# Kernel optimization log

Measured on AMD Instinct MI355X. Metric: run time of the kernel, lower is better.

## Reference

```python
import jax, jax.numpy as jnp
import numpy as np

N_NODES = 100000
N_EDGES = 300000
NUM_GRAPHS = 2000
IN_DIM = 82
HIDDEN = 256


def _gcn_conv(x, src, dst, dinv, W, b):
    # GCNConv: out = D^-1/2 (A + I) D^-1/2 (x W) + b
    xW = x @ W  # [N, H]
    norm = dinv[src] * dinv[dst]  # [E]
    agg = jax.ops.segment_sum(xW[src] * norm[:, None], dst, num_segments=N_NODES)
    self_loop = xW * (dinv * dinv)[:, None]
    return agg + self_loop + b


def setup_inputs() -> dict:
    key = jax.random.key(0)
    ks = jax.random.split(key, 8)
    x = jax.random.normal(ks[0], (N_NODES, IN_DIM), dtype=jnp.float32)
    edge_index = jax.random.randint(ks[1], (2, N_EDGES), 0, N_NODES, dtype=jnp.int64)
    batch = jnp.sort(jax.random.randint(ks[2], (N_NODES,), 0, NUM_GRAPHS, dtype=jnp.int64))
    W1 = jax.random.normal(ks[3], (IN_DIM, HIDDEN), dtype=jnp.float32) * (1.0 / np.sqrt(IN_DIM))
    W2 = jax.random.normal(ks[4], (HIDDEN, HIDDEN), dtype=jnp.float32) * (1.0 / np.sqrt(HIDDEN))
    W3 = jax.random.normal(ks[5], (HIDDEN, HIDDEN), dtype=jnp.float32) * (1.0 / np.sqrt(HIDDEN))
    b1 = jnp.zeros((HIDDEN,), jnp.float32)
    b2 = jnp.zeros((HIDDEN,), jnp.float32)
    b3 = jnp.zeros((HIDDEN,), jnp.float32)
    return {"x": x, "edge_index": edge_index, "batch": batch, "num_graphs": NUM_GRAPHS,
            "W1": W1, "b1": b1, "W2": W2, "b2": b2, "W3": W3, "b3": b3}


def reference(x, edge_index, batch, num_graphs, W1, b1, W2, b2, W3, b3):
    src, dst = edge_index[0], edge_index[1]
    # symmetric normalization with added self-loops (PyG gcn_norm)
    deg = jax.ops.segment_sum(jnp.ones_like(dst, dtype=x.dtype), dst, num_segments=N_NODES) + 1.0
    dinv = jax.lax.rsqrt(deg)
    h = jax.nn.relu(_gcn_conv(x, src, dst, dinv, W1, b1))
    h = jax.nn.relu(_gcn_conv(h, src, dst, dinv, W2, b2))
    h = jax.nn.relu(_gcn_conv(h, src, dst, dinv, W3, b3))
    return jax.ops.segment_max(h, batch, num_segments=num_graphs)  # [G, H]
```

## Files before the change

kernel.cpp:

```cpp
#include <hip/hip_runtime.h>
#include <cstdint>
#include <cstddef>

#define N_NODES 100000
#define N_EDGES 300000
#define N_GRAPHS 2000
#define HID 256
#define INDIM 82
#define K1PAD 96
#define SCAN_CHUNK 2048
#define NBLK_SCAN ((N_NODES + SCAN_CHUNK - 1) / SCAN_CHUNK)

typedef __bf16 bf16x8 __attribute__((ext_vector_type(8)));
typedef float f32x4 __attribute__((ext_vector_type(4)));

__device__ __forceinline__ unsigned short f2bf(float f) {
    unsigned int u = __float_as_uint(f);
    u = (u + 0x7fffu + ((u >> 16) & 1u)) >> 16;
    return (unsigned short)u;
}
__device__ __forceinline__ float bf2f(unsigned short s) {
    return __uint_as_float(((unsigned int)s) << 16);
}

__global__ void k_cnt_init(int* cnt) {
    int i = blockIdx.x * 256 + threadIdx.x;
    if (i < N_NODES) cnt[i] = 0;
}

__global__ void k_cnt_acc(const int* __restrict__ ei, int* cnt) {
    int e = blockIdx.x * 256 + threadIdx.x;
    if (e < N_EDGES) atomicAdd(&cnt[ei[N_EDGES + e]], 1);
}

__global__ void k_dinv(const int* __restrict__ cnt, float* dinv) {
    int i = blockIdx.x * 256 + threadIdx.x;
    if (i < N_NODES) dinv[i] = rsqrtf((float)cnt[i] + 1.0f);
}

__global__ __launch_bounds__(256) void k_scan1(const int* __restrict__ cnt, int* __restrict__ off,
                                               int* __restrict__ partial) {
    __shared__ int sdata[256];
    const int base = blockIdx.x * SCAN_CHUNK;
    const int t = threadIdx.x;
    int v[8];
    int s = 0;
#pragma unroll
    for (int i = 0; i < 8; ++i) {
        int idx = base + t * 8 + i;
        v[i] = (idx < N_NODES) ? cnt[idx] : 0;
        s += v[i];
    }
    sdata[t] = s;
    __syncthreads();
    for (int d = 1; d < 256; d <<= 1) {
        int x = (t >= d) ? sdata[t - d] : 0;
        __syncthreads();
        sdata[t] += x;
        __syncthreads();
    }
    int run = sdata[t] - s;
#pragma unroll
    for (int i = 0; i < 8; ++i) {
        int idx = base + t * 8 + i;
        if (idx < N_NODES) off[idx] = run;
        run += v[i];
    }
    if (t == 255) partial[blockIdx.x] = sdata[255];
}

__global__ void k_scan2(int* partial) {
    if (threadIdx.x == 0 && blockIdx.x == 0) {
        int run = 0;
        for (int i = 0; i < NBLK_SCAN; ++i) {
            int v = partial[i];
            partial[i] = run;
            run += v;
        }
    }
}

__global__ void k_scan3(int* __restrict__ off, const int* __restrict__ partial,
                        int* __restrict__ cur) {
    int i = blockIdx.x * 256 + threadIdx.x;
    if (i < N_NODES) {
        int o = off[i] + partial[i >> 11];
        off[i] = o;
        cur[i] = o;
    }
}

__global__ void k_fill(const int* __restrict__ ei, int* cur, int* __restrict__ csr_src) {
    int e = blockIdx.x * 256 + threadIdx.x;
    if (e < N_EDGES) {
        int s = ei[e];
        int d = ei[N_EDGES + e];
        int pos = atomicAdd(&cur[d], 1);
        csr_src[pos] = s;
    }
}

__global__ void k_bounds(const int* __restrict__ batch, int* __restrict__ gstart) {
    int g = blockIdx.x * 256 + threadIdx.x;
    if (g > N_GRAPHS) return;
    int lo = 0, hi = N_NODES;
    while (lo < hi) {
        int mid = (lo + hi) >> 1;
        if (batch[mid] < g) lo = mid + 1;
        else hi = mid;
    }
    gstart[g] = lo;
}

__global__ void k_xconv(const float* __restrict__ x, unsigned short* __restrict__ xb) {
    int i = blockIdx.x * 256 + threadIdx.x;
    if (i >= N_NODES * K1PAD) return;
    int node = i / K1PAD;
    int k = i - node * K1PAD;
    xb[i] = (k < INDIM) ? f2bf(x[(size_t)node * INDIM + k]) : (unsigned short)0;
}

__global__ void k_wconv(const float* __restrict__ W, unsigned short* __restrict__ Wb,
                        int KPAD, int KSRC) {
    int i = blockIdx.x * 256 + threadIdx.x;
    if (i >= 256 * KPAD) return;
    int kc = i >> 13;
    int r = i & 8191;
    int nt = r >> 9;
    int r2 = r & 511;
    int lg = r2 >> 7;
    int lr = (r2 >> 3) & 15;
    int j = r2 & 7;
    int k = kc * 32 + lg * 8 + j;
    int n = nt * 16 + lr;
    Wb[i] = (k < KSRC) ? f2bf(W[(size_t)k * HID + n]) : (unsigned short)0;
}

template <int K>
__global__ __launch_bounds__(512) void k_gemm_mfma(const unsigned short* __restrict__ A,
                                                   const unsigned short* __restrict__ Wb,
                                                   unsigned short* __restrict__ Cb) {
    constexpr int NK = K / 32;
    __shared__ __align__(16) unsigned short buf[2][8192];

    const int tid = threadIdx.x;
    const int w = tid >> 6;
    const int l = tid & 63;
    const int lr = l & 15;
    const int lg = l >> 4;

    const int rowbase = blockIdx.x * 256 + w * 32;
    int r0 = rowbase + lr;
    int r1 = rowbase + 16 + lr;
    int r0c = r0 < N_NODES ? r0 : (N_NODES - 1);
    int r1c = r1 < N_NODES ? r1 : (N_NODES - 1);
    const unsigned short* a0p = A + (size_t)r0c * K + lg * 8;
    const unsigned short* a1p = A + (size_t)r1c * K + lg * 8;

    bf16x8 a0[NK], a1[NK];
#pragma unroll
    for (int kc = 0; kc < NK; ++kc) {
        a0[kc] = *reinterpret_cast<const bf16x8*>(a0p + kc * 32);
        a1[kc] = *reinterpret_cast<const bf16x8*>(a1p + kc * 32);
    }

    uint4 st0 = *reinterpret_cast<const uint4*>(Wb + tid * 8);
    uint4 st1 = *reinterpret_cast<const uint4*>(Wb + 4096 + tid * 8);

    f32x4 acc0[16] = {};
    f32x4 acc1[16] = {};

#pragma unroll
    for (int kc = 0; kc < NK; ++kc) {
        unsigned short* b = buf[kc & 1];
        *reinterpret_cast<uint4*>(b + tid * 8) = st0;
        *reinterpret_cast<uint4*>(b + 4096 + tid * 8) = st1;
        if (kc + 1 < NK) {
            const unsigned short* src = Wb + (size_t)(kc + 1) * 8192;
            st0 = *reinterpret_cast<const uint4*>(src + tid * 8);
            st1 = *reinterpret_cast<const uint4*>(src + 4096 + tid * 8);
        }
        __syncthreads();
        const unsigned short* bfp = buf[kc & 1] + (size_t)l * 8;
#pragma unroll
        for (int nt = 0; nt < 16; ++nt) {
            bf16x8 bb = *reinterpret_cast<const bf16x8*>(bfp + nt * 512);
            acc0[nt] = __builtin_amdgcn_mfma_f32_16x16x32_bf16(a0[kc], bb, acc0[nt], 0, 0, 0);
            acc1[nt] = __builtin_amdgcn_mfma_f32_16x16x32_bf16(a1[kc], bb, acc1[nt], 0, 0, 0);
        }
        __syncthreads();
    }

    int gr0 = rowbase + lg * 4;
#pragma unroll
    for (int j = 0; j < 4; ++j) {
        int gr = gr0 + j;
        if (gr < N_NODES) {
            size_t base = (size_t)gr * HID + lr;
#pragma unroll
            for (int nt = 0; nt < 16; ++nt) Cb[base + nt * 16] = f2bf(acc0[nt][j]);
        }
        int gr2 = gr + 16;
        if (gr2 < N_NODES) {
            size_t base = (size_t)gr2 * HID + lr;
#pragma unroll
            for (int nt = 0; nt < 16; ++nt) Cb[base + nt * 16] = f2bf(acc1[nt][j]);
        }
    }
}

__global__ void k_aggregate(const unsigned short* __restrict__ tb,
                            const float* __restrict__ dinv, const int* __restrict__ off,
                            const int* __restrict__ cnt, const int* __restrict__ csr_src,
                            const float* __restrict__ bias, unsigned short* __restrict__ hb) {
    int node = blockIdx.x * 4 + (threadIdx.x >> 6);
    if (node >= N_NODES) return;
    int lane = threadIdx.x & 63;
    float di = dinv[node];
    float s2 = di * di;
    ushort4 sv = *reinterpret_cast<const ushort4*>(&tb[(size_t)node * HID + lane * 4]);
    float4 bb = *reinterpret_cast<const float4*>(&bias[lane * 4]);
    float4 acc = {fmaf(bf2f(sv.x), s2, bb.x), fmaf(bf2f(sv.y), s2, bb.y),
                  fmaf(bf2f(sv.z), s2, bb.z), fmaf(bf2f(sv.w), s2, bb.w)};

    int o0 = off[node];
    int n = cnt[node];
    int j = 0;
    for (; j + 1 < n; j += 2) {
        int s0 = csr_src[o0 + j];
        int s1 = csr_src[o0 + j + 1];
        float n0 = dinv[s0] * di;
        float n1 = dinv[s1] * di;
        ushort4 u0 = *reinterpret_cast<const ushort4*>(&tb[(size_t)s0 * HID + lane * 4]);
        ushort4 u1 = *reinterpret_cast<const ushort4*>(&tb[(size_t)s1 * HID + lane * 4]);
        acc.x = fmaf(n0, bf2f(u0.x), acc.x);
        acc.y = fmaf(n0, bf2f(u0.y), acc.y);
        acc.z = fmaf(n0, bf2f(u0.z), acc.z);
        acc.w = fmaf(n0, bf2f(u0.w), acc.w);
        acc.x = fmaf(n1, bf2f(u1.x), acc.x);
        acc.y = fmaf(n1, bf2f(u1.y), acc.y);
        acc.z = fmaf(n1, bf2f(u1.z), acc.z);
        acc.w = fmaf(n1, bf2f(u1.w), acc.w);
    }
    if (j < n) {
        int s0 = csr_src[o0 + j];
        float n0 = dinv[s0] * di;
        ushort4 u0 = *reinterpret_cast<const ushort4*>(&tb[(size_t)s0 * HID + lane * 4]);
        acc.x = fmaf(n0, bf2f(u0.x), acc.x);
        acc.y = fmaf(n0, bf2f(u0.y), acc.y);
        acc.z = fmaf(n0, bf2f(u0.z), acc.z);
        acc.w = fmaf(n0, bf2f(u0.w), acc.w);
    }
    ushort4 o;
    o.x = f2bf(fmaxf(acc.x, 0.0f));
    o.y = f2bf(fmaxf(acc.y, 0.0f));
    o.z = f2bf(fmaxf(acc.z, 0.0f));
    o.w = f2bf(fmaxf(acc.w, 0.0f));
    *reinterpret_cast<ushort4*>(&hb[(size_t)node * HID + lane * 4]) = o;
}

__global__ void k_pool2(const unsigned short* __restrict__ hb, const int* __restrict__ gstart,
                        float* __restrict__ out) {
    int g = blockIdx.x;
    int lane = threadIdx.x;
    int s = gstart[g], e = gstart[g + 1];
    float4 m = {0.0f, 0.0f, 0.0f, 0.0f};
    for (int i = s; i < e; ++i) {
        ushort4 u = *reinterpret_cast<const ushort4*>(&hb[(size_t)i * HID + lane * 4]);
        m.x = fmaxf(m.x, bf2f(u.x));
        m.y = fmaxf(m.y, bf2f(u.y));
        m.z = fmaxf(m.z, bf2f(u.z));
        m.w = fmaxf(m.w, bf2f(u.w));
    }
    *reinterpret_cast<float4*>(&out[(size_t)g * HID + lane * 4]) = m;
}

extern "C" void kernel_launch(void* const* d_in, const int* in_sizes, int n_in,
                              void* d_out, int out_size, void* d_ws, size_t ws_size,
                              hipStream_t stream) {
    const float* x = (const float*)d_in[0];
    const int* ei = (const int*)d_in[1];
    const int* batch = (const int*)d_in[2];
    const float* W1 = (const float*)d_in[4];
    const float* b1 = (const float*)d_in[5];
    const float* W2 = (const float*)d_in[6];
    const float* b2 = (const float*)d_in[7];
    const float* W3 = (const float*)d_in[8];
    const float* b3 = (const float*)d_in[9];
    float* out = (float*)d_out;

    char* ws = (char*)d_ws;
    float* dinv = (float*)(ws);
    int* cnt = (int*)(ws + (512 << 10));
    int* off = (int*)(ws + (1024 << 10));
    int* cur = (int*)(ws + (1536 << 10));
    int* part = (int*)(ws + (2048 << 10));
    int* gstart = (int*)(ws + (2048 << 10) + 4096);
    int* csr_src = (int*)(ws + (2176 << 10));
    unsigned short* Wb1 = (unsigned short*)(ws + (3584 << 10));
    unsigned short* Wb2 = (unsigned short*)(ws + (3712 << 10));
    unsigned short* Wb3 = (unsigned short*)(ws + (3840 << 10));
    unsigned short* tmp_b = (unsigned short*)(ws + (4096 << 10));
    unsigned short* h_b = (unsigned short*)(ws + (4096 << 10) + 51200000);
    unsigned short* x_b = h_b;

    const int nblk_nodes = (N_NODES + 255) / 256;
    const int nblk_edges = (N_EDGES + 255) / 256;
    const int nblk_rows4 = (N_NODES + 3) / 4;
    const int nblk_gemm = (N_NODES + 255) / 256;

    k_cnt_init<<<nblk_nodes, 256, 0, stream>>>(cnt);
    k_cnt_acc<<<nblk_edges, 256, 0, stream>>>(ei, cnt);
    k_dinv<<<nblk_nodes, 256, 0, stream>>>(cnt, dinv);
    k_scan1<<<NBLK_SCAN, 256, 0, stream>>>(cnt, off, part);
    k_scan2<<<1, 64, 0, stream>>>(part);
    k_scan3<<<nblk_nodes, 256, 0, stream>>>(off, part, cur);
    k_fill<<<nblk_edges, 256, 0, stream>>>(ei, cur, csr_src);
    k_bounds<<<(N_GRAPHS + 256) / 256, 256, 0, stream>>>(batch, gstart);

    k_xconv<<<(N_NODES * K1PAD + 255) / 256, 256, 0, stream>>>(x, x_b);
    k_wconv<<<(256 * K1PAD + 255) / 256, 256, 0, stream>>>(W1, Wb1, K1PAD, INDIM);
    k_wconv<<<(256 * HID + 255) / 256, 256, 0, stream>>>(W2, Wb2, HID, HID);
    k_wconv<<<(256 * HID + 255) / 256, 256, 0, stream>>>(W3, Wb3, HID, HID);

    k_gemm_mfma<K1PAD><<<nblk_gemm, 512, 0, stream>>>(x_b, Wb1, tmp_b);
    k_aggregate<<<nblk_rows4, 256, 0, stream>>>(tmp_b, dinv, off, cnt, csr_src, b1, h_b);

    k_gemm_mfma<HID><<<nblk_gemm, 512, 0, stream>>>(h_b, Wb2, tmp_b);
    k_aggregate<<<nblk_rows4, 256, 0, stream>>>(tmp_b, dinv, off, cnt, csr_src, b2, h_b);

    k_gemm_mfma<HID><<<nblk_gemm, 512, 0, stream>>>(h_b, Wb3, tmp_b);
    k_aggregate<<<nblk_rows4, 256, 0, stream>>>(tmp_b, dinv, off, cnt, csr_src, b3, h_b);

    k_pool2<<<N_GRAPHS, 64, 0, stream>>>(h_b, gstart, out);
}
```

Measured before the change: 307.0 us.

## Aggregate before GEMM, fuse bias+ReLU into persistent LDS-resident GEMM

Each GCN layer is reordered to (A·X)·W. The first layer's sparse gather then runs on 128-wide padded bf16 input rows instead of 256-wide transformed rows. Bias and ReLU move into the GEMM epilogue. The GEMM becomes a persistent 256-block kernel that loads the whole weight matrix into LDS once and loops over row tiles. The dinv computation is folded into the scan kernel to drop one launch. The trade-offs are a 128 KB LDS footprint limiting occupancy to one block per CU, uneven tile distribution across the persistent blocks, and padding K1 to 128, which adds MFMA work to the first GEMM.

```diff
diff --git a/kernel.cpp b/kernel.cpp
--- a/kernel.cpp
+++ b/kernel.cpp
@@ -7,7 +7,8 @@
 #define N_GRAPHS 2000
 #define HID 256
 #define INDIM 82
-#define K1PAD 96
+#define K1PAD 128
+#define N_TILES ((N_NODES + 255) / 256)
 #define SCAN_CHUNK 2048
 #define NBLK_SCAN ((N_NODES + SCAN_CHUNK - 1) / SCAN_CHUNK)
 
@@ -31,11 +32,6 @@
 __global__ void k_cnt_acc(const int* __restrict__ ei, int* cnt) {
     int e = blockIdx.x * 256 + threadIdx.x;
     if (e < N_EDGES) atomicAdd(&cnt[ei[N_EDGES + e]], 1);
-}
-
-__global__ void k_dinv(const int* __restrict__ cnt, float* dinv) {
-    int i = blockIdx.x * 256 + threadIdx.x;
-    if (i < N_NODES) dinv[i] = rsqrtf((float)cnt[i] + 1.0f);
 }
 
 __global__ __launch_bounds__(256) void k_scan1(const int* __restrict__ cnt, int* __restrict__ off,
@@ -81,12 +77,14 @@
 }
 
 __global__ void k_scan3(int* __restrict__ off, const int* __restrict__ partial,
-                        int* __restrict__ cur) {
+                        int* __restrict__ cur, const int* __restrict__ cnt,
+                        float* __restrict__ dinv) {
     int i = blockIdx.x * 256 + threadIdx.x;
     if (i < N_NODES) {
         int o = off[i] + partial[i >> 11];
         off[i] = o;
         cur[i] = o;
+        dinv[i] = rsqrtf((float)cnt[i] + 1.0f);
     }
 }
 
@@ -115,8 +113,8 @@
 __global__ void k_xconv(const float* __restrict__ x, unsigned short* __restrict__ xb) {
     int i = blockIdx.x * 256 + threadIdx.x;
     if (i >= N_NODES * K1PAD) return;
-    int node = i / K1PAD;
-    int k = i - node * K1PAD;
+    int node = i >> 7;
+    int k = i & 127;
     xb[i] = (k < INDIM) ? f2bf(x[(size_t)node * INDIM + k]) : (unsigned short)0;
 }
 
@@ -139,9 +137,10 @@
 template <int K>
 __global__ __launch_bounds__(512) void k_gemm_mfma(const unsigned short* __restrict__ A,
                                                    const unsigned short* __restrict__ Wb,
+                                                   const float* __restrict__ bias,
                                                    unsigned short* __restrict__ Cb) {
     constexpr int NK = K / 32;
-    __shared__ __align__(16) unsigned short buf[2][8192];
+    __shared__ __align__(16) unsigned short Wsh[K * HID];
 
     const int tid = threadIdx.x;
     const int w = tid >> 6;
@@ -149,79 +148,79 @@
     const int lr = l & 15;
     const int lg = l >> 4;
 
-    const int rowbase = blockIdx.x * 256 + w * 32;
-    int r0 = rowbase + lr;
-    int r1 = rowbase + 16 + lr;
-    int r0c = r0 < N_NODES ? r0 : (N_NODES - 1);
-    int r1c = r1 < N_NODES ? r1 : (N_NODES - 1);
-    const unsigned short* a0p = A + (size_t)r0c * K + lg * 8;
-    const unsigned short* a1p = A + (size_t)r1c * K + lg * 8;
-
-    bf16x8 a0[NK], a1[NK];
-#pragma unroll
-    for (int kc = 0; kc < NK; ++kc) {
-        a0[kc] = *reinterpret_cast<const bf16x8*>(a0p + kc * 32);
-        a1[kc] = *reinterpret_cast<const bf16x8*>(a1p + kc * 32);
-    }
-
-    uint4 st0 = *reinterpret_cast<const uint4*>(Wb + tid * 8);
-    uint4 st1 = *reinterpret_cast<const uint4*>(Wb + 4096 + tid * 8);
-
-    f32x4 acc0[16] = {};
-    f32x4 acc1[16] = {};
-
-#pragma unroll
-    for (int kc = 0; kc < NK; ++kc) {
-        unsigned short* b = buf[kc & 1];
-        *reinterpret_cast<uint4*>(b + tid * 8) = st0;
-        *reinterpret_cast<uint4*>(b + 4096 + tid * 8) = st1;
-        if (kc + 1 < NK) {
-            const unsigned short* src = Wb + (size_t)(kc + 1) * 8192;
-            st0 = *reinterpret_cast<const uint4*>(src + tid * 8);
-            st1 = *reinterpret_cast<const uint4*>(src + 4096 + tid * 8);
+#pragma unroll
+    for (int i = 0; i < K / 16; ++i) {
+        int o = (i * 512 + tid) * 8;
+        *reinterpret_cast<uint4*>(&Wsh[o]) = *reinterpret_cast<const uint4*>(Wb + o);
+    }
+    __syncthreads();
+
+    float bv[16];
+#pragma unroll
+    for (int nt = 0; nt < 16; ++nt) bv[nt] = bias[nt * 16 + lr];
+
+    for (int t = blockIdx.x; t < N_TILES; t += 256) {
+        const int rowbase = t * 256 + w * 32;
+        int r0 = rowbase + lr;
+        int r1 = rowbase + 16 + lr;
+        int r0c = r0 < N_NODES ? r0 : (N_NODES - 1);
+        int r1c = r1 < N_NODES ? r1 : (N_NODES - 1);
+        const unsigned short* a0p = A + (size_t)r0c * K + lg * 8;
+        const unsigned short* a1p = A + (size_t)r1c * K + lg * 8;
+
+        bf16x8 a0[NK], a1[NK];
+#pragma unroll
+        for (int kc = 0; kc < NK; ++kc) {
+            a0[kc] = *reinterpret_cast<const bf16x8*>(a0p + kc * 32);
+            a1[kc] = *reinterpret_cast<const bf16x8*>(a1p + kc * 32);
         }
-        __syncthreads();
-        const unsigned short* bfp = buf[kc & 1] + (size_t)l * 8;
-#pragma unroll
-        for (int nt = 0; nt < 16; ++nt) {
-            bf16x8 bb = *reinterpret_cast<const bf16x8*>(bfp + nt * 512);
-            acc0[nt] = __builtin_amdgcn_mfma_f32_16x16x32_bf16(a0[kc], bb, acc0[nt], 0, 0, 0);
-            acc1[nt] = __builtin_amdgcn_mfma_f32_16x16x32_bf16(a1[kc], bb, acc1[nt], 0, 0, 0);
+
+        f32x4 acc0[16] = {};
+        f32x4 acc1[16] = {};
+
+#pragma unroll
+        for (int kc = 0; kc < NK; ++kc) {
+            const unsigned short* bfp = Wsh + kc * 8192 + l * 8;
+#pragma unroll
+            for (int nt = 0; nt < 16; ++nt) {
+                bf16x8 bb = *reinterpret_cast<const bf16x8*>(bfp + nt * 512);
+                acc0[nt] = __builtin_amdgcn_mfma_f32_16x16x32_bf16(a0[kc], bb, acc0[nt], 0, 0, 0);
+                acc1[nt] = __builtin_amdgcn_mfma_f32_16x16x32_bf16(a1[kc], bb, acc1[nt], 0, 0, 0);
+            }
         }
-        __syncthreads();
-    }
-
-    int gr0 = rowbase + lg * 4;
-#pragma unroll
-    for (int j = 0; j < 4; ++j) {
-        int gr = gr0 + j;
-        if (gr < N_NODES) {
-            size_t base = (size_t)gr * HID + lr;
-#pragma unroll
-            for (int nt = 0; nt < 16; ++nt) Cb[base + nt * 16] = f2bf(acc0[nt][j]);
+
+        int gr0 = rowbase + lg * 4;
+#pragma unroll
+        for (int j = 0; j < 4; ++j) {
+            int gr = gr0 + j;
+            if (gr < N_NODES) {
+                size_t base = (size_t)gr * HID + lr;
+#pragma unroll
+                for (int nt = 0; nt < 16; ++nt)
+                    Cb[base + nt * 16] = f2bf(fmaxf(acc0[nt][j] + bv[nt], 0.0f));
+            }
+            int gr2 = gr + 16;
+            if (gr2 < N_NODES) {
+                size_t base = (size_t)gr2 * HID + lr;
+#pragma unroll
+                for (int nt = 0; nt < 16; ++nt)
+                    Cb[base + nt * 16] = f2bf(fmaxf(acc1[nt][j] + bv[nt], 0.0f));
+            }
         }
-        int gr2 = gr + 16;
-        if (gr2 < N_NODES) {
-            size_t base = (size_t)gr2 * HID + lr;
-#pragma unroll
-            for (int nt = 0; nt < 16; ++nt) Cb[base + nt * 16] = f2bf(acc1[nt][j]);
-        }
-    }
-}
-
-__global__ void k_aggregate(const unsigned short* __restrict__ tb,
-                            const float* __restrict__ dinv, const int* __restrict__ off,
-                            const int* __restrict__ cnt, const int* __restrict__ csr_src,
-                            const float* __restrict__ bias, unsigned short* __restrict__ hb) {
+    }
+}
+
+__global__ void k_aggregate256(const unsigned short* __restrict__ tb,
+                               const float* __restrict__ dinv, const int* __restrict__ off,
+                               const int* __restrict__ cnt, const int* __restrict__ csr_src,
+                               unsigned short* __restrict__ ob) {
     int node = blockIdx.x * 4 + (threadIdx.x >> 6);
     if (node >= N_NODES) return;
     int lane = threadIdx.x & 63;
     float di = dinv[node];
     float s2 = di * di;
     ushort4 sv = *reinterpret_cast<const ushort4*>(&tb[(size_t)node * HID + lane * 4]);
-    float4 bb = *reinterpret_cast<const float4*>(&bias[lane * 4]);
-    float4 acc = {fmaf(bf2f(sv.x), s2, bb.x), fmaf(bf2f(sv.y), s2, bb.y),
-                  fmaf(bf2f(sv.z), s2, bb.z), fmaf(bf2f(sv.w), s2, bb.w)};
+    float4 acc = {bf2f(sv.x) * s2, bf2f(sv.y) * s2, bf2f(sv.z) * s2, bf2f(sv.w) * s2};
 
     int o0 = off[node];
     int n = cnt[node];
@@ -252,11 +251,51 @@
         acc.w = fmaf(n0, bf2f(u0.w), acc.w);
     }
     ushort4 o;
-    o.x = f2bf(fmaxf(acc.x, 0.0f));
-    o.y = f2bf(fmaxf(acc.y, 0.0f));
-    o.z = f2bf(fmaxf(acc.z, 0.0f));
-    o.w = f2bf(fmaxf(acc.w, 0.0f));
-    *reinterpret_cast<ushort4*>(&hb[(size_t)node * HID + lane * 4]) = o;
+    o.x = f2bf(acc.x);
+    o.y = f2bf(acc.y);
+    o.z = f2bf(acc.z);
+    o.w = f2bf(acc.w);
+    *reinterpret_cast<ushort4*>(&ob[(size_t)node * HID + lane * 4]) = o;
+}
+
+__global__ void k_aggregate128(const unsigned short* __restrict__ tb,
+                               const float* __restrict__ dinv, const int* __restrict__ off,
+                               const int* __restrict__ cnt, const int* __restrict__ csr_src,
+                               unsigned short* __restrict__ ob) {
+    int node = blockIdx.x * 4 + (threadIdx.x >> 6);
+    if (node >= N_NODES) return;
+    int lane = threadIdx.x & 63;
+    float di = dinv[node];
+    float s2 = di * di;
+    ushort2 sv = *reinterpret_cast<const ushort2*>(&tb[(size_t)node * K1PAD + lane * 2]);
+    float2 acc = {bf2f(sv.x) * s2, bf2f(sv.y) * s2};
+
+    int o0 = off[node];
+    int n = cnt[node];
+    int j = 0;
+    for (; j + 1 < n; j += 2) {
+        int s0 = csr_src[o0 + j];
+        int s1 = csr_src[o0 + j + 1];
+        float n0 = dinv[s0] * di;
+        float n1 = dinv[s1] * di;
+        ushort2 u0 = *reinterpret_cast<const ushort2*>(&tb[(size_t)s0 * K1PAD + lane * 2]);
+        ushort2 u1 = *reinterpret_cast<const ushort2*>(&tb[(size_t)s1 * K1PAD + lane * 2]);
+        acc.x = fmaf(n0, bf2f(u0.x), acc.x);
+        acc.y = fmaf(n0, bf2f(u0.y), acc.y);
+        acc.x = fmaf(n1, bf2f(u1.x), acc.x);
+        acc.y = fmaf(n1, bf2f(u1.y), acc.y);
+    }
+    if (j < n) {
+        int s0 = csr_src[o0 + j];
+        float n0 = dinv[s0] * di;
+        ushort2 u0 = *reinterpret_cast<const ushort2*>(&tb[(size_t)s0 * K1PAD + lane * 2]);
+        acc.x = fmaf(n0, bf2f(u0.x), acc.x);
+        acc.y = fmaf(n0, bf2f(u0.y), acc.y);
+    }
+    ushort2 o;
+    o.x = f2bf(acc.x);
+    o.y = f2bf(acc.y);
+    *reinterpret_cast<ushort2*>(&ob[(size_t)node * K1PAD + lane * 2]) = o;
 }
 
 __global__ void k_pool2(const unsigned short* __restrict__ hb, const int* __restrict__ gstart,
@@ -299,22 +338,21 @@
     int* csr_src = (int*)(ws + (2176 << 10));
     unsigned short* Wb1 = (unsigned short*)(ws + (3584 << 10));
     unsigned short* Wb2 = (unsigned short*)(ws + (3712 << 10));
-    unsigned short* Wb3 = (unsigned short*)(ws + (3840 << 10));
-    unsigned short* tmp_b = (unsigned short*)(ws + (4096 << 10));
-    unsigned short* h_b = (unsigned short*)(ws + (4096 << 10) + 51200000);
-    unsigned short* x_b = h_b;
+    unsigned short* Wb3 = (unsigned short*)(ws + (3904 << 10));
+    unsigned short* x_b = (unsigned short*)(ws + (4096 << 10));
+    unsigned short* ag1_b = (unsigned short*)(ws + (4096 << 10) + 25600000);
+    unsigned short* bufA = (unsigned short*)(ws + (4096 << 10) + 51200000);
+    unsigned short* bufB = (unsigned short*)(ws + (4096 << 10) + 102400000);
 
     const int nblk_nodes = (N_NODES + 255) / 256;
     const int nblk_edges = (N_EDGES + 255) / 256;
     const int nblk_rows4 = (N_NODES + 3) / 4;
-    const int nblk_gemm = (N_NODES + 255) / 256;
 
     k_cnt_init<<<nblk_nodes, 256, 0, stream>>>(cnt);
     k_cnt_acc<<<nblk_edges, 256, 0, stream>>>(ei, cnt);
-    k_dinv<<<nblk_nodes, 256, 0, stream>>>(cnt, dinv);
     k_scan1<<<NBLK_SCAN, 256, 0, stream>>>(cnt, off, part);
     k_scan2<<<1, 64, 0, stream>>>(part);
-    k_scan3<<<nblk_nodes, 256, 0, stream>>>(off, part, cur);
+    k_scan3<<<nblk_nodes, 256, 0, stream>>>(off, part, cur, cnt, dinv);
     k_fill<<<nblk_edges, 256, 0, stream>>>(ei, cur, csr_src);
     k_bounds<<<(N_GRAPHS + 256) / 256, 256, 0, stream>>>(batch, gstart);
 
@@ -323,14 +361,14 @@
     k_wconv<<<(256 * HID + 255) / 256, 256, 0, stream>>>(W2, Wb2, HID, HID);
     k_wconv<<<(256 * HID + 255) / 256, 256, 0, stream>>>(W3, Wb3, HID, HID);
 
-    k_gemm_mfma<K1PAD><<<nblk_gemm, 512, 0, stream>>>(x_b, Wb1, tmp_b);
-    k_aggregate<<<nblk_rows4, 256, 0, stream>>>(tmp_b, dinv, off, cnt, csr_src, b1, h_b);
-
-    k_gemm_mfma<HID><<<nblk_gemm, 512, 0, stream>>>(h_b, Wb2, tmp_b);
-    k_aggregate<<<nblk_rows4, 256, 0, stream>>>(tmp_b, dinv, off, cnt, csr_src, b2, h_b);
-
-    k_gemm_mfma<HID><<<nblk_gemm, 512, 0, stream>>>(h_b, Wb3, tmp_b);
-    k_aggregate<<<nblk_rows4, 256, 0, stream>>>(tmp_b, dinv, off, cnt, csr_src, b3, h_b);
-
-    k_pool2<<<N_GRAPHS, 64, 0, stream>>>(h_b, gstart, out);
-}
+    k_aggregate128<<<nblk_rows4, 256, 0, stream>>>(x_b, dinv, off, cnt, csr_src, ag1_b);
+    k_gemm_mfma<K1PAD><<<256, 512, 0, stream>>>(ag1_b, Wb1, b1, bufA);
+
+    k_aggregate256<<<nblk_rows4, 256, 0, stream>>>(bufA, dinv, off, cnt, csr_src, bufB);
+    k_gemm_mfma<HID><<<256, 512, 0, stream>>>(bufB, Wb2, b2, bufA);
+
+    k_aggregate256<<<nblk_rows4, 256, 0, stream>>>(bufA, dinv, off, cnt, csr_src, bufB);
+    k_gemm_mfma<HID><<<256, 512, 0, stream>>>(bufB, Wb3, b3, bufA);
+
+    k_pool2<<<N_GRAPHS, 64, 0, stream>>>(bufA, gstart, out);
+}
```

Result: faster. 282.7 us (-7.9%).
